# Performance work log

Measured on AMD Instinct MI355X. Metric: run time of the kernel, lower is better.

The kernel has to match this reference:

```python
import jax, jax.numpy as jnp
import numpy as np

N, E, F_IN, H, G, C, L = 100000, 1600000, 128, 128, 1000, 10, 3
EPS = 1e-5


def setup_inputs() -> dict:
    key = jax.random.key(0)
    ks = jax.random.split(key, 10)
    x = jax.random.normal(ks[0], (N, F_IN), dtype=jnp.float32)
    edge_index = jax.random.randint(ks[1], (2, E), 0, N, dtype=jnp.int64)
    batch = jnp.sort(jax.random.randint(ks[2], (N,), 0, G, dtype=jnp.int64))
    s = 1.0 / np.sqrt(H)
    conv_w = jax.random.normal(ks[3], (L, F_IN, H), dtype=jnp.float32) * s
    conv_b = jnp.zeros((L, H), dtype=jnp.float32)
    bn_gamma = jnp.ones((L, H), dtype=jnp.float32)
    bn_beta = jnp.zeros((L, H), dtype=jnp.float32)
    w1 = jax.random.normal(ks[4], (H, H // 2), dtype=jnp.float32) * s
    b1 = jnp.zeros((H // 2,), dtype=jnp.float32)
    w2 = jax.random.normal(ks[5], (H // 2, C), dtype=jnp.float32) * (1.0 / np.sqrt(H // 2))
    b2 = jnp.zeros((C,), dtype=jnp.float32)
    return {"x": x, "conv_w": conv_w, "conv_b": conv_b, "bn_gamma": bn_gamma,
            "bn_beta": bn_beta, "w1": w1, "b1": b1, "w2": w2, "b2": b2,
            "edge_index": edge_index, "batch": batch}


def _gcn_conv(x, w, b, src, dst):
    # PyG GCNConv: h = x @ W; symmetric-normalized aggregation with self-loops.
    h = x @ w  # [N, H]
    deg = 1.0 + jax.ops.segment_sum(jnp.ones((E,), x.dtype), dst, num_segments=N)
    dinv = jax.lax.rsqrt(deg)  # [N]
    norm = dinv[src] * dinv[dst]  # [E]
    agg = jax.ops.segment_sum(h[src] * norm[:, None], dst, num_segments=N)
    agg = agg + h * (dinv * dinv)[:, None]  # self-loop contribution
    return agg + b


def _batchnorm(x, gamma, beta):
    mean = jnp.mean(x, axis=0)
    var = jnp.mean(jnp.square(x - mean), axis=0)  # biased, as in torch BN fwd
    return gamma * (x - mean) * jax.lax.rsqrt(var + EPS) + beta


def reference(x, conv_w, conv_b, bn_gamma, bn_beta, w1, b1, w2, b2, edge_index, batch):
    src, dst = edge_index[0], edge_index[1]
    h = x
    for i in range(L):
        h = _gcn_conv(h, conv_w[i], conv_b[i], src, dst)
        h = _batchnorm(h, bn_gamma[i], bn_beta[i])
        h = jax.nn.relu(h)  # dropout is identity in eval mode
    # global mean pool over graphs
    sums = jax.ops.segment_sum(h, batch, num_segments=G)
    cnts = jax.ops.segment_sum(jnp.ones((N,), h.dtype), batch, num_segments=G)
    pooled = sums / jnp.maximum(cnts, 1.0)[:, None]
    # classifier MLP
    z = jax.nn.relu(pooled @ w1 + b1)
    return z @ w2 + b2
```

## Files before the change

kernel.cpp:

```cpp
#include <hip/hip_runtime.h>
#include <hip/hip_bf16.h>

#define N_NODES 100000
#define N_EDGES 1600000
#define HDIM    128
#define NGRAPH  1000
#define NCLASS  10
#define BN_EPS  1e-5f

#define BSHIFT  7
#define BMASK   127
#define NBUCKET 782
#define TILE3   8192
#define NSB     196
#define GATHER_BLOCKS 1024

typedef short short8_t __attribute__((ext_vector_type(8)));
typedef float f32x4_t  __attribute__((ext_vector_type(4)));

__device__ __forceinline__ float bf2f(ushort u) {
    union { unsigned int i; float f; } v; v.i = ((unsigned int)u) << 16; return v.f;
}
__device__ __forceinline__ ushort f2bf(float f) {
    union { float f; unsigned int i; } v; v.f = f;
    unsigned int i = v.i;
    unsigned int r = i + 0x7fffu + ((i >> 16) & 1u);
    return (ushort)(r >> 16);
}
__device__ __forceinline__ unsigned int pack2(float a, float b) {
    return (unsigned int)f2bf(a) | ((unsigned int)f2bf(b) << 16);
}
__device__ __forceinline__ float lo16(unsigned int u) {
    union { unsigned int i; float f; } v; v.i = u << 16; return v.f;
}
__device__ __forceinline__ float hi16(unsigned int u) {
    union { unsigned int i; float f; } v; v.i = u & 0xffff0000u; return v.f;
}

__global__ __launch_bounds__(256)
void wprep_hist(const float* __restrict__ W, ushort* __restrict__ wtbT,
                const int* __restrict__ dst, int* __restrict__ blockhist) {
    __shared__ int h[NBUCKET];
    int t = threadIdx.x;
    if (blockIdx.x < 48) {
        int l = blockIdx.x >> 4, slice = blockIdx.x & 15;
        int idx = slice * 1024 + t * 4;
        int k = idx >> 7, n = idx & 127;
        float4 w4 = *(const float4*)&W[(size_t)l * 16384 + k * 128 + n];
        ushort* o = wtbT + (size_t)l * 16384;
        o[(n + 0) * 128 + k] = f2bf(w4.x);
        o[(n + 1) * 128 + k] = f2bf(w4.y);
        o[(n + 2) * 128 + k] = f2bf(w4.z);
        o[(n + 3) * 128 + k] = f2bf(w4.w);
        return;
    }
    int blk = blockIdx.x - 48;
    for (int i = t; i < NBUCKET; i += 256) h[i] = 0;
    __syncthreads();
    long tile0 = (long)blk * TILE3;
    #pragma unroll 4
    for (int i = 0; i < TILE3 / 256; i++) {
        long e = tile0 + t + i * 256;
        if (e < N_EDGES) atomicAdd(&h[dst[e] >> BSHIFT], 1);
    }
    __syncthreads();
    for (int b = t; b < NBUCKET; b += 256)
        blockhist[(size_t)b * NSB + blk] = h[b];
}

__global__ __launch_bounds__(64)
void col_scan(int* __restrict__ blockhist, int* __restrict__ coltotal) {
    int b = blockIdx.x * 64 + threadIdx.x;
    if (b >= NBUCKET) return;
    int s = 0;
    for (int blk = 0; blk < NSB; blk++) {
        int v = blockhist[(size_t)b * NSB + blk];
        blockhist[(size_t)b * NSB + blk] = s;
        s += v;
    }
    coltotal[b] = s;
}

__global__ __launch_bounds__(1024)
void bucket_scan(const int* __restrict__ coltotal, int* __restrict__ bucket_base,
                 int* __restrict__ row_start) {
    __shared__ int wsum[16];
    int t = threadIdx.x, lane = t & 63, wid = t >> 6;
    int v = (t < NBUCKET) ? coltotal[t] : 0;
    int x = v;
    #pragma unroll
    for (int off = 1; off < 64; off <<= 1) {
        int y = __shfl_up(x, off, 64);
        if (lane >= off) x += y;
    }
    if (lane == 63) wsum[wid] = x;
    __syncthreads();
    if (t == 0) {
        int s = 0;
        #pragma unroll
        for (int w = 0; w < 16; w++) { int tmp = wsum[w]; wsum[w] = s; s += tmp; }
    }
    __syncthreads();
    int excl = wsum[wid] + (x - v);
    if (t < NBUCKET) bucket_base[t] = excl;
    if (t == 0) { bucket_base[NBUCKET] = N_EDGES; row_start[N_NODES] = N_EDGES; }
}

__global__ __launch_bounds__(256)
void scatter_pairs(const int* __restrict__ src, const int* __restrict__ dst,
                   const int* __restrict__ bucket_base, const int* __restrict__ blockhist,
                   unsigned int* __restrict__ pairs) {
    __shared__ int lbase[NBUCKET];
    __shared__ int lcur[NBUCKET];
    int t = threadIdx.x;
    int blk = blockIdx.x;
    for (int b = t; b < NBUCKET; b += 256) {
        lbase[b] = bucket_base[b] + blockhist[(size_t)b * NSB + blk];
        lcur[b] = 0;
    }
    __syncthreads();
    long tile0 = (long)blk * TILE3;
    #pragma unroll 4
    for (int i = 0; i < TILE3 / 256; i++) {
        long e = tile0 + t + i * 256;
        if (e < N_EDGES) {
            int d = dst[e];
            int bkt = d >> BSHIFT;
            int p = atomicAdd(&lcur[bkt], 1);
            pairs[lbase[bkt] + p] = (unsigned int)src[e] | ((unsigned int)(d & BMASK) << 24);
        }
    }
}

__global__ __launch_bounds__(256)
void build_csr(const unsigned int* __restrict__ pairs, const int* __restrict__ bucket_base,
               int* __restrict__ row_start, int* __restrict__ csr_src, float* __restrict__ dinv) {
    __shared__ int hist[128];
    __shared__ int cur[128];
    __shared__ int wsum[2];
    int b = blockIdx.x;
    int t = threadIdx.x;
    int beg = bucket_base[b], end = bucket_base[b + 1];
    if (t < 128) hist[t] = 0;
    __syncthreads();
    for (int e = beg + t; e < end; e += 256)
        atomicAdd(&hist[pairs[e] >> 24], 1);
    __syncthreads();
    int v = 0, x = 0;
    int lane = t & 63, wid = t >> 6;
    if (t < 128) {
        v = hist[t];
        x = v;
        #pragma unroll
        for (int off = 1; off < 64; off <<= 1) {
            int y = __shfl_up(x, off, 64);
            if (lane >= off) x += y;
        }
        if (lane == 63) wsum[wid] = x;
    }
    __syncthreads();
    if (t == 0) { int s = wsum[0]; wsum[0] = 0; wsum[1] = s; }
    __syncthreads();
    if (t < 128) {
        int excl = wsum[wid] + (x - v);
        cur[t] = excl;
        int node = b * 128 + t;
        if (node < N_NODES) {
            row_start[node] = beg + excl;
            dinv[node] = rsqrtf(1.0f + (float)v);
        }
    }
    __syncthreads();
    for (int e = beg + t; e < end; e += 256) {
        unsigned int pk = pairs[e];
        int ln = pk >> 24;
        int sp = atomicAdd(&cur[ln], 1);
        csr_src[beg + sp] = (int)(pk & 0xFFFFFFu);
    }
}

__global__ __launch_bounds__(256)
void gemm_mfma(const float* __restrict__ inf, const ushort* __restrict__ inb,
               const ushort* __restrict__ wtbT, const float* __restrict__ bnp,
               const float* __restrict__ dinv, ushort* __restrict__ out) {
    __shared__ ushort as_[64][136];
    __shared__ ushort wt[128][136];
    int t = threadIdx.x;
    int wave = t >> 6, lane = t & 63;
    int g = lane >> 4, c = lane & 15;
    int rowbase = blockIdx.x * 64;

    #pragma unroll
    for (int i = 0; i < 8; i++) {
        int cid = t + i * 256;
        int n = cid >> 4, ko = (cid & 15) * 8;
        uint4 v = *(const uint4*)&wtbT[n * 128 + ko];
        *(uint4*)&wt[n][ko] = v;
    }
    if (inf) {
        #pragma unroll
        for (int i = 0; i < 8; i++) {
            int cid = t + i * 256;
            int r = cid >> 5, co = (cid & 31) * 4;
            int row = rowbase + r;
            ushort4 pk = make_ushort4(0, 0, 0, 0);
            if (row < N_NODES) {
                float4 v = *(const float4*)&inf[(size_t)row * HDIM + co];
                pk.x = f2bf(v.x); pk.y = f2bf(v.y); pk.z = f2bf(v.z); pk.w = f2bf(v.w);
            }
            *(ushort4*)&as_[r][co] = pk;
        }
    } else {
        #pragma unroll
        for (int i = 0; i < 4; i++) {
            int cid = t + i * 256;
            int r = cid >> 4, co = (cid & 15) * 8;
            int row = rowbase + r;
            uint4 o = make_uint4(0, 0, 0, 0);
            if (row < N_NODES) {
                uint4 p = *(const uint4*)&inb[(size_t)row * HDIM + co];
                float4 scA = *(const float4*)&bnp[co];
                float4 scB = *(const float4*)&bnp[co + 4];
                float4 shA = *(const float4*)&bnp[128 + co];
                float4 shB = *(const float4*)&bnp[132 + co];
                float v0 = fmaxf(0.f, fmaf(lo16(p.x), scA.x, shA.x));
                float v1 = fmaxf(0.f, fmaf(hi16(p.x), scA.y, shA.y));
                float v2 = fmaxf(0.f, fmaf(lo16(p.y), scA.z, shA.z));
                float v3 = fmaxf(0.f, fmaf(hi16(p.y), scA.w, shA.w));
                float v4 = fmaxf(0.f, fmaf(lo16(p.z), scB.x, shB.x));
                float v5 = fmaxf(0.f, fmaf(hi16(p.z), scB.y, shB.y));
                float v6 = fmaxf(0.f, fmaf(lo16(p.w), scB.z, shB.z));
                float v7 = fmaxf(0.f, fmaf(hi16(p.w), scB.w, shB.w));
                o.x = pack2(v0, v1); o.y = pack2(v2, v3);
                o.z = pack2(v4, v5); o.w = pack2(v6, v7);
            }
            *(uint4*)&as_[r][co] = o;
        }
    }
    __syncthreads();

    int m0 = wave * 16;
    short8_t a[4];
    #pragma unroll
    for (int ch = 0; ch < 4; ch++)
        a[ch] = *(const short8_t*)&as_[m0 + c][ch * 32 + g * 8];
    f32x4_t acc[8] = {};
    #pragma unroll
    for (int ct = 0; ct < 8; ct++) {
        #pragma unroll
        for (int ch = 0; ch < 4; ch++) {
            short8_t b = *(const short8_t*)&wt[ct * 16 + c][ch * 32 + g * 8];
            acc[ct] = __builtin_amdgcn_mfma_f32_16x16x32_bf16(a[ch], b, acc[ct], 0, 0, 0);
        }
    }
    float dv[4];
    #pragma unroll
    for (int reg = 0; reg < 4; reg++) {
        int rr = rowbase + m0 + g * 4 + reg;
        dv[reg] = dinv[rr < N_NODES ? rr : 0];
    }
    __syncthreads();
    #pragma unroll
    for (int ct = 0; ct < 8; ct++)
        #pragma unroll
        for (int reg = 0; reg < 4; reg++)
            as_[m0 + g * 4 + reg][ct * 16 + c] = f2bf(acc[ct][reg] * dv[reg]);
    __syncthreads();
    #pragma unroll
    for (int i = 0; i < 8; i++) {
        int cid = t + i * 256;
        int r = cid >> 5, co = (cid & 31) * 4;
        int row = rowbase + r;
        if (row < N_NODES)
            *(ushort4*)&out[(size_t)row * HDIM + co] = *(const ushort4*)&as_[r][co];
    }
}

__global__ __launch_bounds__(256)
void gather_agg(const ushort* __restrict__ hw, const int* __restrict__ row_start,
                const int* __restrict__ csr_src, const float* __restrict__ dinv,
                const float* __restrict__ bias, ushort* __restrict__ aggout,
                float* __restrict__ Spart, float* __restrict__ Qpart) {
    __shared__ float s_sum[128];
    __shared__ float s_sq[128];
    int t = threadIdx.x;
    if (t < 128) { s_sum[t] = 0.f; s_sq[t] = 0.f; }
    __syncthreads();
    int lane = t & 63, wid = t >> 6;
    int g = lane >> 4, c = lane & 15;
    int fo = c * 8;
    float4 bA = *(const float4*)&bias[fo];
    float4 bB = *(const float4*)&bias[fo + 4];
    float ls[8] = {}, lq[8] = {};
    int gw = blockIdx.x * 4 + wid;
    int nw = gridDim.x * 4;
    for (int n = gw; n < N_NODES; n += nw) {
        int jb = row_start[n], je = row_start[n + 1];
        float acc[8] = {};
        int j = jb;
        for (; j + 16 <= je; j += 16) {
            int s0 = csr_src[j + 4 * g + 0];
            int s1 = csr_src[j + 4 * g + 1];
            int s2 = csr_src[j + 4 * g + 2];
            int s3 = csr_src[j + 4 * g + 3];
            uint4 p0 = *(const uint4*)&hw[(size_t)s0 * HDIM + fo];
            uint4 p1 = *(const uint4*)&hw[(size_t)s1 * HDIM + fo];
            uint4 p2 = *(const uint4*)&hw[(size_t)s2 * HDIM + fo];
            uint4 p3 = *(const uint4*)&hw[(size_t)s3 * HDIM + fo];
            acc[0] += (lo16(p0.x) + lo16(p1.x)) + (lo16(p2.x) + lo16(p3.x));
            acc[1] += (hi16(p0.x) + hi16(p1.x)) + (hi16(p2.x) + hi16(p3.x));
            acc[2] += (lo16(p0.y) + lo16(p1.y)) + (lo16(p2.y) + lo16(p3.y));
            acc[3] += (hi16(p0.y) + hi16(p1.y)) + (hi16(p2.y) + hi16(p3.y));
            acc[4] += (lo16(p0.z) + lo16(p1.z)) + (lo16(p2.z) + lo16(p3.z));
            acc[5] += (hi16(p0.z) + hi16(p1.z)) + (hi16(p2.z) + hi16(p3.z));
            acc[6] += (lo16(p0.w) + lo16(p1.w)) + (lo16(p2.w) + lo16(p3.w));
            acc[7] += (hi16(p0.w) + hi16(p1.w)) + (hi16(p2.w) + hi16(p3.w));
        }
        for (; j + 8 <= je; j += 8) {
            int sa = csr_src[j + 2 * g];
            int sb = csr_src[j + 2 * g + 1];
            uint4 p = *(const uint4*)&hw[(size_t)sa * HDIM + fo];
            uint4 q = *(const uint4*)&hw[(size_t)sb * HDIM + fo];
            acc[0] += lo16(p.x) + lo16(q.x);
            acc[1] += hi16(p.x) + hi16(q.x);
            acc[2] += lo16(p.y) + lo16(q.y);
            acc[3] += hi16(p.y) + hi16(q.y);
            acc[4] += lo16(p.z) + lo16(q.z);
            acc[5] += hi16(p.z) + hi16(q.z);
            acc[6] += lo16(p.w) + lo16(q.w);
            acc[7] += hi16(p.w) + hi16(q.w);
        }
        int e0 = j + g, e1 = j + 4 + g;
        if (e0 < je) {
            int s = csr_src[e0];
            uint4 p = *(const uint4*)&hw[(size_t)s * HDIM + fo];
            acc[0] += lo16(p.x); acc[1] += hi16(p.x);
            acc[2] += lo16(p.y); acc[3] += hi16(p.y);
            acc[4] += lo16(p.z); acc[5] += hi16(p.z);
            acc[6] += lo16(p.w); acc[7] += hi16(p.w);
        }
        if (e1 < je) {
            int s = csr_src[e1];
            uint4 p = *(const uint4*)&hw[(size_t)s * HDIM + fo];
            acc[0] += lo16(p.x); acc[1] += hi16(p.x);
            acc[2] += lo16(p.y); acc[3] += hi16(p.y);
            acc[4] += lo16(p.z); acc[5] += hi16(p.z);
            acc[6] += lo16(p.w); acc[7] += hi16(p.w);
        }
        #pragma unroll
        for (int i = 0; i < 8; i++) {
            acc[i] += __shfl_xor(acc[i], 16);
            acc[i] += __shfl_xor(acc[i], 32);
        }
        uint4 ps = *(const uint4*)&hw[(size_t)n * HDIM + fo];
        float dn = dinv[n];
        float r[8];
        r[0] = fmaf(acc[0] + lo16(ps.x), dn, bA.x);
        r[1] = fmaf(acc[1] + hi16(ps.x), dn, bA.y);
        r[2] = fmaf(acc[2] + lo16(ps.y), dn, bA.z);
        r[3] = fmaf(acc[3] + hi16(ps.y), dn, bA.w);
        r[4] = fmaf(acc[4] + lo16(ps.z), dn, bB.x);
        r[5] = fmaf(acc[5] + hi16(ps.z), dn, bB.y);
        r[6] = fmaf(acc[6] + lo16(ps.w), dn, bB.z);
        r[7] = fmaf(acc[7] + hi16(ps.w), dn, bB.w);
        if (g == 0) {
            uint4 o;
            o.x = pack2(r[0], r[1]); o.y = pack2(r[2], r[3]);
            o.z = pack2(r[4], r[5]); o.w = pack2(r[6], r[7]);
            *(uint4*)&aggout[(size_t)n * HDIM + fo] = o;
            #pragma unroll
            for (int i = 0; i < 8; i++) { ls[i] += r[i]; lq[i] += r[i] * r[i]; }
        }
    }
    if (g == 0) {
        #pragma unroll
        for (int i = 0; i < 8; i++) {
            atomicAdd(&s_sum[fo + i], ls[i]);
            atomicAdd(&s_sq[fo + i],  lq[i]);
        }
    }
    __syncthreads();
    if (t < 128) {
        Spart[(size_t)blockIdx.x * 128 + t] = s_sum[t];
        Qpart[(size_t)blockIdx.x * 128 + t] = s_sq[t];
    }
}

__global__ __launch_bounds__(256)
void bn_reduce_prep(const float* __restrict__ Spart, const float* __restrict__ Qpart,
                    const float* __restrict__ gamma, const float* __restrict__ beta,
                    float* __restrict__ bnp) {
    __shared__ float rs[32][8];
    __shared__ float rq[32][8];
    int t = threadIdx.x;
    int fi = t & 7, chunk = t >> 3;
    int f = blockIdx.x * 8 + fi;
    float s = 0.f, q = 0.f;
    for (int b = chunk; b < GATHER_BLOCKS; b += 32) {
        s += Spart[(size_t)b * 128 + f];
        q += Qpart[(size_t)b * 128 + f];
    }
    rs[chunk][fi] = s; rq[chunk][fi] = q;
    __syncthreads();
    if (t < 8) {
        float S = 0.f, Q = 0.f;
        #pragma unroll
        for (int cc = 0; cc < 32; cc++) { S += rs[cc][t]; Q += rq[cc][t]; }
        int ff = blockIdx.x * 8 + t;
        float mean = S * (1.0f / N_NODES);
        float var  = Q * (1.0f / N_NODES) - mean * mean;
        float inv  = rsqrtf(var + BN_EPS);
        float sc   = gamma[ff] * inv;
        bnp[ff]       = sc;
        bnp[128 + ff] = beta[ff] - mean * sc;
    }
}

__global__ __launch_bounds__(128)
void pool_mlp(const ushort* __restrict__ agg, const float* __restrict__ bnp,
              const int* __restrict__ batch, const float* __restrict__ w1,
              const float* __restrict__ b1, const float* __restrict__ w2,
              const float* __restrict__ b2, float* __restrict__ out) {
    __shared__ float p[128];
    __shared__ float z[64];
    int g = blockIdx.x;
    int k = threadIdx.x;
    int lo = 0, hi = N_NODES;
    while (lo < hi) { int mid = (lo + hi) >> 1; if (batch[mid] < g) lo = mid + 1; else hi = mid; }
    int start = lo;
    hi = N_NODES;
    while (lo < hi) { int mid = (lo + hi) >> 1; if (batch[mid] < g + 1) lo = mid + 1; else hi = mid; }
    int end = lo;
    float sc = bnp[k], sh = bnp[128 + k];
    float sum = 0.f;
    int n = start;
    for (; n + 4 <= end; n += 4) {
        float a0 = bf2f(agg[(size_t)(n + 0) * HDIM + k]);
        float a1 = bf2f(agg[(size_t)(n + 1) * HDIM + k]);
        float a2 = bf2f(agg[(size_t)(n + 2) * HDIM + k]);
        float a3 = bf2f(agg[(size_t)(n + 3) * HDIM + k]);
        sum += fmaxf(0.f, fmaf(a0, sc, sh));
        sum += fmaxf(0.f, fmaf(a1, sc, sh));
        sum += fmaxf(0.f, fmaf(a2, sc, sh));
        sum += fmaxf(0.f, fmaf(a3, sc, sh));
    }
    for (; n < end; n++)
        sum += fmaxf(0.f, fmaf(bf2f(agg[(size_t)n * HDIM + k]), sc, sh));
    float cnt = (float)(end - start);
    p[k] = sum / fmaxf(cnt, 1.0f);
    __syncthreads();
    if (k < 64) {
        float s = b1[k];
        #pragma unroll 8
        for (int kk = 0; kk < 128; kk++) s += p[kk] * w1[kk * 64 + k];
        z[k] = fmaxf(0.f, s);
    }
    __syncthreads();
    if (k < NCLASS) {
        float s = b2[k];
        #pragma unroll
        for (int j = 0; j < 64; j++) s += z[j] * w2[j * NCLASS + k];
        out[g * NCLASS + k] = s;
    }
}

extern "C" void kernel_launch(void* const* d_in, const int* in_sizes, int n_in,
                              void* d_out, int out_size, void* d_ws, size_t ws_size,
                              hipStream_t stream) {
    const float* x      = (const float*)d_in[0];
    const float* conv_w = (const float*)d_in[1];
    const float* conv_b = (const float*)d_in[2];
    const float* gamma  = (const float*)d_in[3];
    const float* beta   = (const float*)d_in[4];
    const float* w1     = (const float*)d_in[5];
    const float* b1     = (const float*)d_in[6];
    const float* w2     = (const float*)d_in[7];
    const float* b2     = (const float*)d_in[8];
    const int*   ei     = (const int*)d_in[9];
    const int*   batch  = (const int*)d_in[10];
    float* out = (float*)d_out;

    char* ws = (char*)d_ws;
    size_t off = 0;
    auto alloc = [&](size_t bytes) -> void* {
        off = (off + 255) & ~(size_t)255;
        void* p = ws + off;
        off += bytes;
        return p;
    };
    ushort* A         = (ushort*)alloc((size_t)N_NODES * HDIM * 2);
    ushort* aggB      = (ushort*)alloc((size_t)N_NODES * HDIM * 2);
    int*    csr_src   = (int*)   alloc((size_t)N_EDGES * 4);
    int*    row_start = (int*)   alloc((size_t)(N_NODES + 1) * 4);
    float*  dinv      = (float*) alloc((size_t)N_NODES * 4);
    int*    blockhist = (int*)   alloc((size_t)NBUCKET * NSB * 4);
    int*    coltotal  = (int*)   alloc((size_t)NBUCKET * 4);
    int*    bbase     = (int*)   alloc((size_t)(NBUCKET + 1) * 4);
    ushort* wtbT      = (ushort*)alloc((size_t)3 * 16384 * 2);
    float*  Spart     = (float*) alloc((size_t)GATHER_BLOCKS * 128 * 4);
    float*  Qpart     = (float*) alloc((size_t)GATHER_BLOCKS * 128 * 4);
    float*  bnp       = (float*) alloc(3 * 256 * 4);
    unsigned int* pairs = (unsigned int*)aggB;

    const int* srcv = ei;
    const int* dstv = ei + N_EDGES;

    wprep_hist   <<<48 + NSB, 256, 0, stream>>>(conv_w, wtbT, dstv, blockhist);
    col_scan     <<<(NBUCKET + 63) / 64, 64, 0, stream>>>(blockhist, coltotal);
    bucket_scan  <<<1, 1024, 0, stream>>>(coltotal, bbase, row_start);
    scatter_pairs<<<NSB, 256, 0, stream>>>(srcv, dstv, bbase, blockhist, pairs);
    build_csr    <<<NBUCKET, 256, 0, stream>>>(pairs, bbase, row_start, csr_src, dinv);

    for (int l = 0; l < 3; l++) {
        gemm_mfma<<<(N_NODES + 63) / 64, 256, 0, stream>>>(
            (l == 0) ? x : nullptr, (l == 0) ? nullptr : aggB,
            wtbT + (size_t)l * 16384,
            (l == 0) ? nullptr : (bnp + (l - 1) * 256), dinv, A);
        gather_agg<<<GATHER_BLOCKS, 256, 0, stream>>>(A, row_start, csr_src, dinv,
                                                      conv_b + l * HDIM, aggB, Spart, Qpart);
        bn_reduce_prep<<<16, 256, 0, stream>>>(Spart, Qpart, gamma + l * HDIM,
                                               beta + l * HDIM, bnp + l * 256);
    }
    pool_mlp<<<NGRAPH, 128, 0, stream>>>(aggB, bnp + 2 * 256, batch, w1, b1, w2, b2, out);
}
```

Before: 502.9 us.

## Fuse BN reduction into gather via last-block atomics, parallelize column scan

Drops the separate bn_reduce_prep launch per layer. Each gather block now atomically adds its partial sums into 16 slot buffers, and the last block to finish, found through an atomic counter, computes the BN scale and shift. The column scan moves from one serial thread per bucket to one wave per bucket using shuffle prefix sums, and csr_src loads become nontemporal. This saves three kernel launches and some serial scan latency, in exchange for contended float atomics and a threadfence in every gather block.

```diff
diff --git a/kernel.cpp b/kernel.cpp
--- a/kernel.cpp
+++ b/kernel.cpp
@@ -70,20 +70,29 @@
 
 __global__ __launch_bounds__(64)
 void col_scan(int* __restrict__ blockhist, int* __restrict__ coltotal) {
-    int b = blockIdx.x * 64 + threadIdx.x;
-    if (b >= NBUCKET) return;
-    int s = 0;
-    for (int blk = 0; blk < NSB; blk++) {
-        int v = blockhist[(size_t)b * NSB + blk];
-        blockhist[(size_t)b * NSB + blk] = s;
-        s += v;
-    }
-    coltotal[b] = s;
+    int b = blockIdx.x;
+    int lane = threadIdx.x;
+    int base = b * NSB;
+    int carry = 0;
+    for (int r = 0; r < NSB; r += 64) {
+        int i = r + lane;
+        int v = (i < NSB) ? blockhist[base + i] : 0;
+        int x = v;
+        #pragma unroll
+        for (int off = 1; off < 64; off <<= 1) {
+            int y = __shfl_up(x, off, 64);
+            if (lane >= off) x += y;
+        }
+        if (i < NSB) blockhist[base + i] = carry + x - v;
+        carry += __shfl(x, 63, 64);
+    }
+    if (lane == 0) coltotal[b] = carry;
 }
 
 __global__ __launch_bounds__(1024)
 void bucket_scan(const int* __restrict__ coltotal, int* __restrict__ bucket_base,
-                 int* __restrict__ row_start) {
+                 int* __restrict__ row_start, float* __restrict__ slotbuf,
+                 int* __restrict__ counters) {
     __shared__ int wsum[16];
     int t = threadIdx.x, lane = t & 63, wid = t >> 6;
     int v = (t < NBUCKET) ? coltotal[t] : 0;
@@ -104,6 +113,8 @@
     int excl = wsum[wid] + (x - v);
     if (t < NBUCKET) bucket_base[t] = excl;
     if (t == 0) { bucket_base[NBUCKET] = N_EDGES; row_start[N_NODES] = N_EDGES; }
+    for (int i = t; i < 3 * 2 * 16 * 128; i += 1024) slotbuf[i] = 0.f;
+    if (t < 3) counters[t] = 0;
 }
 
 __global__ __launch_bounds__(256)
@@ -280,9 +291,12 @@
 void gather_agg(const ushort* __restrict__ hw, const int* __restrict__ row_start,
                 const int* __restrict__ csr_src, const float* __restrict__ dinv,
                 const float* __restrict__ bias, ushort* __restrict__ aggout,
-                float* __restrict__ Spart, float* __restrict__ Qpart) {
+                float* __restrict__ slotS, float* __restrict__ slotQ,
+                int* __restrict__ counter, const float* __restrict__ gamma,
+                const float* __restrict__ beta, float* __restrict__ bnp) {
     __shared__ float s_sum[128];
     __shared__ float s_sq[128];
+    __shared__ int isLast;
     int t = threadIdx.x;
     if (t < 128) { s_sum[t] = 0.f; s_sq[t] = 0.f; }
     __syncthreads();
@@ -299,10 +313,10 @@
         float acc[8] = {};
         int j = jb;
         for (; j + 16 <= je; j += 16) {
-            int s0 = csr_src[j + 4 * g + 0];
-            int s1 = csr_src[j + 4 * g + 1];
-            int s2 = csr_src[j + 4 * g + 2];
-            int s3 = csr_src[j + 4 * g + 3];
+            int s0 = __builtin_nontemporal_load(&csr_src[j + 4 * g + 0]);
+            int s1 = __builtin_nontemporal_load(&csr_src[j + 4 * g + 1]);
+            int s2 = __builtin_nontemporal_load(&csr_src[j + 4 * g + 2]);
+            int s3 = __builtin_nontemporal_load(&csr_src[j + 4 * g + 3]);
             uint4 p0 = *(const uint4*)&hw[(size_t)s0 * HDIM + fo];
             uint4 p1 = *(const uint4*)&hw[(size_t)s1 * HDIM + fo];
             uint4 p2 = *(const uint4*)&hw[(size_t)s2 * HDIM + fo];
@@ -317,8 +331,8 @@
             acc[7] += (hi16(p0.w) + hi16(p1.w)) + (hi16(p2.w) + hi16(p3.w));
         }
         for (; j + 8 <= je; j += 8) {
-            int sa = csr_src[j + 2 * g];
-            int sb = csr_src[j + 2 * g + 1];
+            int sa = __builtin_nontemporal_load(&csr_src[j + 2 * g]);
+            int sb = __builtin_nontemporal_load(&csr_src[j + 2 * g + 1]);
             uint4 p = *(const uint4*)&hw[(size_t)sa * HDIM + fo];
             uint4 q = *(const uint4*)&hw[(size_t)sb * HDIM + fo];
             acc[0] += lo16(p.x) + lo16(q.x);
@@ -380,39 +394,27 @@
         }
     }
     __syncthreads();
+    int slot = (blockIdx.x & 15) * 128;
     if (t < 128) {
-        Spart[(size_t)blockIdx.x * 128 + t] = s_sum[t];
-        Qpart[(size_t)blockIdx.x * 128 + t] = s_sq[t];
-    }
-}
-
-__global__ __launch_bounds__(256)
-void bn_reduce_prep(const float* __restrict__ Spart, const float* __restrict__ Qpart,
-                    const float* __restrict__ gamma, const float* __restrict__ beta,
-                    float* __restrict__ bnp) {
-    __shared__ float rs[32][8];
-    __shared__ float rq[32][8];
-    int t = threadIdx.x;
-    int fi = t & 7, chunk = t >> 3;
-    int f = blockIdx.x * 8 + fi;
-    float s = 0.f, q = 0.f;
-    for (int b = chunk; b < GATHER_BLOCKS; b += 32) {
-        s += Spart[(size_t)b * 128 + f];
-        q += Qpart[(size_t)b * 128 + f];
-    }
-    rs[chunk][fi] = s; rq[chunk][fi] = q;
-    __syncthreads();
-    if (t < 8) {
-        float S = 0.f, Q = 0.f;
-        #pragma unroll
-        for (int cc = 0; cc < 32; cc++) { S += rs[cc][t]; Q += rq[cc][t]; }
-        int ff = blockIdx.x * 8 + t;
-        float mean = S * (1.0f / N_NODES);
-        float var  = Q * (1.0f / N_NODES) - mean * mean;
-        float inv  = rsqrtf(var + BN_EPS);
-        float sc   = gamma[ff] * inv;
-        bnp[ff]       = sc;
-        bnp[128 + ff] = beta[ff] - mean * sc;
+        atomicAdd(&slotS[slot + t], s_sum[t]);
+        atomicAdd(&slotQ[slot + t], s_sq[t]);
+    }
+    __threadfence();
+    if (t == 0) isLast = (atomicAdd(counter, 1) == GATHER_BLOCKS - 1);
+    __syncthreads();
+    if (isLast) {
+        __threadfence();
+        if (t < 128) {
+            float S = 0.f, Q = 0.f;
+            #pragma unroll
+            for (int s = 0; s < 16; s++) { S += slotS[s * 128 + t]; Q += slotQ[s * 128 + t]; }
+            float mean = S * (1.0f / N_NODES);
+            float var  = Q * (1.0f / N_NODES) - mean * mean;
+            float inv  = rsqrtf(var + BN_EPS);
+            float sc   = gamma[t] * inv;
+            bnp[t]       = sc;
+            bnp[128 + t] = beta[t] - mean * sc;
+        }
     }
 }
 
@@ -497,8 +499,8 @@
     int*    coltotal  = (int*)   alloc((size_t)NBUCKET * 4);
     int*    bbase     = (int*)   alloc((size_t)(NBUCKET + 1) * 4);
     ushort* wtbT      = (ushort*)alloc((size_t)3 * 16384 * 2);
-    float*  Spart     = (float*) alloc((size_t)GATHER_BLOCKS * 128 * 4);
-    float*  Qpart     = (float*) alloc((size_t)GATHER_BLOCKS * 128 * 4);
+    float*  slotbuf   = (float*) alloc((size_t)3 * 2 * 16 * 128 * 4);
+    int*    counters  = (int*)   alloc(3 * 4);
     float*  bnp       = (float*) alloc(3 * 256 * 4);
     unsigned int* pairs = (unsigned int*)aggB;
 
@@ -506,8 +508,8 @@
     const int* dstv = ei + N_EDGES;
 
     wprep_hist   <<<48 + NSB, 256, 0, stream>>>(conv_w, wtbT, dstv, blockhist);
-    col_scan     <<<(NBUCKET + 63) / 64, 64, 0, stream>>>(blockhist, coltotal);
-    bucket_scan  <<<1, 1024, 0, stream>>>(coltotal, bbase, row_start);
+    col_scan     <<<NBUCKET, 64, 0, stream>>>(blockhist, coltotal);
+    bucket_scan  <<<1, 1024, 0, stream>>>(coltotal, bbase, row_start, slotbuf, counters);
     scatter_pairs<<<NSB, 256, 0, stream>>>(srcv, dstv, bbase, blockhist, pairs);
     build_csr    <<<NBUCKET, 256, 0, stream>>>(pairs, bbase, row_start, csr_src, dinv);
 
@@ -516,10 +518,10 @@
             (l == 0) ? x : nullptr, (l == 0) ? nullptr : aggB,
             wtbT + (size_t)l * 16384,
             (l == 0) ? nullptr : (bnp + (l - 1) * 256), dinv, A);
-        gather_agg<<<GATHER_BLOCKS, 256, 0, stream>>>(A, row_start, csr_src, dinv,
-                                                      conv_b + l * HDIM, aggB, Spart, Qpart);
-        bn_reduce_prep<<<16, 256, 0, stream>>>(Spart, Qpart, gamma + l * HDIM,
-                                               beta + l * HDIM, bnp + l * 256);
+        gather_agg<<<GATHER_BLOCKS, 256, 0, stream>>>(
+            A, row_start, csr_src, dinv, conv_b + l * HDIM, aggB,
+            slotbuf + (size_t)l * 4096, slotbuf + (size_t)l * 4096 + 2048,
+            counters + l, gamma + l * HDIM, beta + l * HDIM, bnp + l * 256);
     }
     pool_mlp<<<NGRAPH, 128, 0, stream>>>(aggB, bnp + 2 * 256, batch, w1, b1, w2, b2, out);
 }
```

Measured after the change: 718.6 us. 1.43x slower.
